# Optimization experiments

Measured on AMD Instinct MI355X. Metric: run time of the kernel, lower is better.

## Reference

```python
import jax, jax.numpy as jnp
import numpy as np

SATURATION = 1.0


def setup_inputs() -> dict:
    key = jax.random.key(0)
    k1, k2, k3, k4, k5 = jax.random.split(key, 5)
    B, Q, C = 128, 2048, 8
    L, K = 256, 64
    ts = jax.random.normal(k1, (B, Q, C), dtype=jnp.float32)
    shapelets = jax.random.normal(k2, (L, K, C), dtype=jnp.float32)  # stacked ParameterList
    gating = jax.random.normal(k3, (L,), dtype=jnp.float32)
    fc1_w = jax.random.normal(k4, (2, L), dtype=jnp.float32) / np.sqrt(L)
    fc1_b = jax.random.normal(k5, (2,), dtype=jnp.float32) * 0.01
    return {"ts": ts, "shapelets": shapelets, "gating": gating,
            "fc1_w": fc1_w, "fc1_b": fc1_b}


def reference(ts, shapelets, gating, fc1_w, fc1_b):
    # ts: [B, Q, C]; shapelets: [L, K, C]
    ts = ts.astype(jnp.float32)
    L, K, C = shapelets.shape
    # ||segment||^2 summed over (K, C) via sliding-window cumsum trick -> [B, S]
    ts2 = jnp.sum(ts * ts, axis=2)                     # [B, Q]
    csum = jnp.pad(jnp.cumsum(ts2, axis=1), ((0, 0), (1, 0)))
    win_sq = csum[:, K:] - csum[:, :-K]                # [B, S], S = Q-K+1
    # cross term <segment, shapelet> for all windows/shapelets via 1D conv
    kernel = jnp.transpose(shapelets, (1, 2, 0))       # [K, C, L] (WIO)
    cross = jax.lax.conv_general_dilated(
        ts, kernel, window_strides=(1,), padding='VALID',
        dimension_numbers=('NWC', 'WIO', 'NWC'))       # [B, S, L]
    sh_sq = jnp.sum(shapelets * shapelets, axis=(1, 2))  # [L]
    # mean squared distance per (batch, window, shapelet)
    dist = (win_sq[:, :, None] - 2.0 * cross + sh_sq[None, None, :]) / (K * C)
    hard_min = jnp.min(dist, axis=1)                   # [B, L] min-pool over windows
    g = jax.nn.sigmoid(SATURATION * gating)            # [L]
    min_dw = hard_min * g                              # equivalent to result @ diag(g)
    return min_dw @ fc1_w.T + fc1_b                    # [B, 2]
```

## Files before the change

kernel.cpp:

```cpp
#include <hip/hip_runtime.h>
#include <stdint.h>

#define B_ 128
#define Q_ 2048
#define C_ 8
#define L_ 256
#define K_ 64
#define S_ 1985
#define KC_ 512
#define BNC_ 64
#define NNT_ 4

typedef short s16x8 __attribute__((ext_vector_type(8)));
typedef float f32x16 __attribute__((ext_vector_type(16)));

__device__ __forceinline__ unsigned short f2bf(float f) {
    unsigned u = __float_as_uint(f);
    u += 0x7FFFu + ((u >> 16) & 1u);
    return (unsigned short)(u >> 16);
}
__device__ __forceinline__ unsigned fenc(float f) {
    unsigned u = __float_as_uint(f);
    return (u & 0x80000000u) ? ~u : (u | 0x80000000u);
}
__device__ __forceinline__ float fdec(unsigned k) {
    unsigned u = (k & 0x80000000u) ? (k ^ 0x80000000u) : ~k;
    return __uint_as_float(u);
}
__device__ __forceinline__ void async_copy16(void* lds_dst, const void* g_src) {
    __builtin_amdgcn_global_load_lds(
        (const __attribute__((address_space(1))) void*)g_src,
        (__attribute__((address_space(3))) void*)lds_dst, 16, 0, 0);
}

__global__ __launch_bounds__(256) void k_prep_ts(const float* __restrict__ ts,
                                                 uint4* __restrict__ tsb,
                                                 unsigned* __restrict__ extg) {
    const int b = blockIdx.x;
    const int t = threadIdx.x;
    __shared__ float t2[2048];
    #pragma unroll
    for (int j = 0; j < 8; ++j) {
        int r = j * 256 + t;
        const float4* p = (const float4*)(ts + ((size_t)b * Q_ + r) * C_);
        float4 x = p[0], y = p[1];
        union { unsigned short h[8]; uint4 v; } u;
        u.h[0] = f2bf(x.x); u.h[1] = f2bf(x.y); u.h[2] = f2bf(x.z); u.h[3] = f2bf(x.w);
        u.h[4] = f2bf(y.x); u.h[5] = f2bf(y.y); u.h[6] = f2bf(y.z); u.h[7] = f2bf(y.w);
        tsb[(size_t)b * Q_ + r] = u.v;
        t2[r] = x.x*x.x + x.y*x.y + x.z*x.z + x.w*x.w
              + y.x*y.x + y.y*y.y + y.z*y.z + y.w*y.w;
    }
    __syncthreads();
    int s0 = t * 8;
    float w = 0.f;
    if (s0 < S_) {
        #pragma unroll 16
        for (int k = 0; k < K_; ++k) w += t2[s0 + k];
    }
    #pragma unroll
    for (int j = 0; j < 8; ++j) {
        int s = s0 + j;
        unsigned word = 0x0000FF80u;
        if (s < S_) {
            float v = -0.5f * w;
            unsigned short hh = f2bf(v);
            float hf = __uint_as_float((unsigned)hh << 16);
            unsigned short ll = f2bf(v - hf);
            word = (unsigned)hh | ((unsigned)ll << 16);
        }
        extg[(size_t)b * Q_ + s] = word;
        if (s + K_ < Q_) w += t2[s + K_] - t2[s];
    }
}

__global__ __launch_bounds__(256) void k_misc(uint4* __restrict__ tsb,
                                              unsigned* __restrict__ hmin) {
    const int bid = blockIdx.x, t = threadIdx.x;
    if (bid < 2) {
        uint4 z; z.x = z.y = z.z = z.w = 0u;
        tsb[B_ * Q_ + bid * 256 + t] = z;
    } else {
        hmin[(bid - 2) * 256 + t] = 0xFFFFFFFFu;
    }
}

__global__ __launch_bounds__(64) void k_prep_sh(const float* __restrict__ sh,
                                                uint4* __restrict__ shb,
                                                float* __restrict__ shsq) {
    const int l = blockIdx.x;
    const int t = threadIdx.x;
    const float4* p = (const float4*)(sh + (size_t)l * KC_) + t * 2;
    float4 x = p[0], y = p[1];
    union { unsigned short h[8]; uint4 v; } u;
    u.h[0] = f2bf(x.x); u.h[1] = f2bf(x.y); u.h[2] = f2bf(x.z); u.h[3] = f2bf(x.w);
    u.h[4] = f2bf(y.x); u.h[5] = f2bf(y.y); u.h[6] = f2bf(y.z); u.h[7] = f2bf(y.w);
    shb[l * 64 + t] = u.v;
    float ss = x.x*x.x + x.y*x.y + x.z*x.z + x.w*x.w
             + y.x*y.x + y.y*y.y + y.z*y.z + y.w*y.w;
    #pragma unroll
    for (int off = 32; off >= 1; off >>= 1) ss += __shfl_down(ss, off, 64);
    if (t == 0) shsq[l] = ss;
}

__global__ __launch_bounds__(256, 2) void k_main(
    const uint4* __restrict__ tsb,
    const char*  __restrict__ shb,
    const unsigned* __restrict__ extg,
    const float* __restrict__ shsq,
    unsigned*    __restrict__ hmin)
{
    __shared__ uint4 b_lds4[4096];
    __shared__ uint4 a_lds4[576];
    __shared__ uint4 e_lds4[128];

    const int nt   = blockIdx.x;
    const int b    = blockIdx.y;
    const int c0   = nt * BNC_;
    const int tid  = threadIdx.x;
    const int lane = tid & 63;
    const int wv   = tid >> 6;
    const int l31  = lane & 31;
    const int hi   = lane >> 5;

    #define STAGE_AE(mi_)                                                      \
        {                                                                      \
            const char* gA = (const char*)(tsb + (size_t)b * Q_ + (mi_) * 512);\
            for (int rr = tid; rr < 576; rr += 256)                            \
                async_copy16((char*)a_lds4 + rr * 16, gA + rr * 16);           \
            if (tid < 128)                                                     \
                async_copy16((char*)e_lds4 + tid * 16,                         \
                             (const char*)(extg + (size_t)b * Q_ + (mi_) * 512)\
                             + tid * 16);                                      \
        }

    #pragma unroll
    for (int it = 0; it < 16; ++it) {
        int col  = wv * 16 + it;
        const char* g = shb + ((size_t)(c0 + col)) * 1024
                      + ((lane ^ (col & 31)) << 4);
        async_copy16((char*)b_lds4 + col * 1024, g);
    }
    STAGE_AE(0)
    __syncthreads();

    const f32x16 fz = {0.f,0.f,0.f,0.f,0.f,0.f,0.f,0.f,
                       0.f,0.f,0.f,0.f,0.f,0.f,0.f,0.f};
    const float inf = __builtin_inff();
    float rm0 = inf, rm1 = inf;

    const char* bb    = (const char*)b_lds4;
    const char* ab    = (const char*)a_lds4;
    const char* eb    = (const char*)e_lds4;
    const int   abase = (wv * 128 + l31 + hi) * 16;
    const int   bcol  = l31 * 1024;

    union UU { unsigned u[4]; s16x8 v; };
    UU be; be.u[0] = hi ? 0u : 0x3F803F80u;
    be.u[1] = 0u; be.u[2] = 0u; be.u[3] = 0u;

    #pragma unroll 1
    for (int mi = 0; mi < 4; ++mi) {
        f32x16 acc00 = fz, acc01 = fz;
        f32x16 acc10 = fz, acc11 = fz;
        f32x16 acc20 = fz, acc21 = fz;
        f32x16 acc30 = fz, acc31 = fz;

        #pragma unroll
        for (int kk = 0; kk < 32; ++kk) {
            s16x8 a0 = *(const s16x8*)(ab + abase + kk * 32);
            s16x8 a1 = *(const s16x8*)(ab + abase + kk * 32 + 512);
            s16x8 a2 = *(const s16x8*)(ab + abase + kk * 32 + 1024);
            s16x8 a3 = *(const s16x8*)(ab + abase + kk * 32 + 1536);
            int ch = (((kk << 1) + hi) ^ l31) << 4;
            s16x8 b0 = *(const s16x8*)(bb + bcol + ch);
            s16x8 b1 = *(const s16x8*)(bb + bcol + ch + 32768);
            __builtin_amdgcn_s_setprio(1);
            acc00 = __builtin_amdgcn_mfma_f32_32x32x16_bf16(a0, b0, acc00, 0, 0, 0);
            acc01 = __builtin_amdgcn_mfma_f32_32x32x16_bf16(a0, b1, acc01, 0, 0, 0);
            acc10 = __builtin_amdgcn_mfma_f32_32x32x16_bf16(a1, b0, acc10, 0, 0, 0);
            acc11 = __builtin_amdgcn_mfma_f32_32x32x16_bf16(a1, b1, acc11, 0, 0, 0);
            acc20 = __builtin_amdgcn_mfma_f32_32x32x16_bf16(a2, b0, acc20, 0, 0, 0);
            acc21 = __builtin_amdgcn_mfma_f32_32x32x16_bf16(a2, b1, acc21, 0, 0, 0);
            acc30 = __builtin_amdgcn_mfma_f32_32x32x16_bf16(a3, b0, acc30, 0, 0, 0);
            acc31 = __builtin_amdgcn_mfma_f32_32x32x16_bf16(a3, b1, acc31, 0, 0, 0);
            __builtin_amdgcn_s_setprio(0);
        }
        {
            unsigned w0 = *(const unsigned*)(eb + (wv * 128 +  0 + l31) * 4);
            unsigned w1 = *(const unsigned*)(eb + (wv * 128 + 32 + l31) * 4);
            unsigned w2 = *(const unsigned*)(eb + (wv * 128 + 64 + l31) * 4);
            unsigned w3 = *(const unsigned*)(eb + (wv * 128 + 96 + l31) * 4);
            UU ae0, ae1, ae2, ae3;
            ae0.u[0] = hi ? 0u : w0; ae0.u[1] = 0; ae0.u[2] = 0; ae0.u[3] = 0;
            ae1.u[0] = hi ? 0u : w1; ae1.u[1] = 0; ae1.u[2] = 0; ae1.u[3] = 0;
            ae2.u[0] = hi ? 0u : w2; ae2.u[1] = 0; ae2.u[2] = 0; ae2.u[3] = 0;
            ae3.u[0] = hi ? 0u : w3; ae3.u[1] = 0; ae3.u[2] = 0; ae3.u[3] = 0;
            acc00 = __builtin_amdgcn_mfma_f32_32x32x16_bf16(ae0.v, be.v, acc00, 0, 0, 0);
            acc01 = __builtin_amdgcn_mfma_f32_32x32x16_bf16(ae0.v, be.v, acc01, 0, 0, 0);
            acc10 = __builtin_amdgcn_mfma_f32_32x32x16_bf16(ae1.v, be.v, acc10, 0, 0, 0);
            acc11 = __builtin_amdgcn_mfma_f32_32x32x16_bf16(ae1.v, be.v, acc11, 0, 0, 0);
            acc20 = __builtin_amdgcn_mfma_f32_32x32x16_bf16(ae2.v, be.v, acc20, 0, 0, 0);
            acc21 = __builtin_amdgcn_mfma_f32_32x32x16_bf16(ae2.v, be.v, acc21, 0, 0, 0);
            acc30 = __builtin_amdgcn_mfma_f32_32x32x16_bf16(ae3.v, be.v, acc30, 0, 0, 0);
            acc31 = __builtin_amdgcn_mfma_f32_32x32x16_bf16(ae3.v, be.v, acc31, 0, 0, 0);
        }
        __syncthreads();
        if (mi < 3) STAGE_AE(mi + 1)

        #define FOLD(accv, rmv)                                                \
            { _Pragma("unroll") for (int r = 0; r < 16; ++r)                   \
                  rmv = fminf(rmv, -2.f * accv[r]); }
        FOLD(acc00, rm0) FOLD(acc10, rm0) FOLD(acc20, rm0) FOLD(acc30, rm0)
        FOLD(acc01, rm1) FOLD(acc11, rm1) FOLD(acc21, rm1) FOLD(acc31, rm1)
        #undef FOLD
        __syncthreads();
    }

    const int colg = c0 + l31;
    rm0 = (rm0 + shsq[colg])      * (1.f / 512.f);
    rm1 = (rm1 + shsq[colg + 32]) * (1.f / 512.f);
    rm0 = fminf(rm0, __shfl_xor(rm0, 32, 64));
    rm1 = fminf(rm1, __shfl_xor(rm1, 32, 64));
    if (hi == 0) {
        atomicMin(&hmin[b * L_ + colg],      fenc(rm0));
        atomicMin(&hmin[b * L_ + colg + 32], fenc(rm1));
    }
}

__global__ __launch_bounds__(256) void k_final(const unsigned* __restrict__ hmin,
                                               const float* __restrict__ gating,
                                               const float* __restrict__ w,
                                               const float* __restrict__ bias,
                                               float* __restrict__ out) {
    const int b = blockIdx.x, t = threadIdx.x;
    float v = fdec(hmin[b * L_ + t]);
    float g = 1.f / (1.f + __expf(-gating[t]));
    float mg = v * g;
    float p0 = mg * w[t];
    float p1 = mg * w[L_ + t];
    #pragma unroll
    for (int off = 32; off >= 1; off >>= 1) {
        p0 += __shfl_down(p0, off, 64);
        p1 += __shfl_down(p1, off, 64);
    }
    __shared__ float r0[4], r1[4];
    int wvi = t >> 6, ln = t & 63;
    if (ln == 0) { r0[wvi] = p0; r1[wvi] = p1; }
    __syncthreads();
    if (t == 0) {
        out[b * 2 + 0] = r0[0] + r0[1] + r0[2] + r0[3] + bias[0];
        out[b * 2 + 1] = r1[0] + r1[1] + r1[2] + r1[3] + bias[1];
    }
}

extern "C" void kernel_launch(void* const* d_in, const int* in_sizes, int n_in,
                              void* d_out, int out_size, void* d_ws, size_t ws_size,
                              hipStream_t stream) {
    const float* ts     = (const float*)d_in[0];
    const float* sh     = (const float*)d_in[1];
    const float* gating = (const float*)d_in[2];
    const float* fw     = (const float*)d_in[3];
    const float* fb     = (const float*)d_in[4];
    float* out = (float*)d_out;

    char* ws = (char*)d_ws;
    uint4*    tsb  = (uint4*)ws;
    char*     shb  = ws + 4202496;
    float*    shsq = (float*)(ws + 4464640);
    unsigned* hmin = (unsigned*)(ws + 4465664);
    unsigned* extg = (unsigned*)(ws + 4596736);

    k_prep_ts<<<128, 256, 0, stream>>>(ts, tsb, extg);
    k_misc<<<130, 256, 0, stream>>>(tsb, hmin);
    k_prep_sh<<<256, 64, 0, stream>>>(sh, (uint4*)shb, shsq);
    dim3 grid(NNT_, B_);
    k_main<<<grid, 256, 0, stream>>>(tsb, shb, extg, shsq, hmin);
    k_final<<<128, 256, 0, stream>>>(hmin, gating, fw, fb, out);
}
```

Baseline: 66.74 us.

## Retile main GEMM, stream shapelets from global, fuse prep kernels

Merges the three prep kernels into a single launch and stores the bf16 shapelets transposed so B fragments can be read straight from global memory. The main kernel's shared-memory B tile is removed. Its tiling changes from 4 column tiles by the full sequence per block to 256-row by 128-column tiles on a 16x128 grid. A double-buffered A tile replaces the old staging, and launch bounds rise to 3 blocks per CU. The aim is less LDS pressure and fewer launches plus higher occupancy, at the risk of extra L2 traffic for B and less reuse per block.

Result: slower. 194.3 us (+191.2%).

```diff
diff --git a/kernel.cpp b/kernel.cpp
--- a/kernel.cpp
+++ b/kernel.cpp
@@ -8,8 +8,6 @@
 #define K_ 64
 #define S_ 1985
 #define KC_ 512
-#define BNC_ 64
-#define NNT_ 4
 
 typedef short s16x8 __attribute__((ext_vector_type(8)));
 typedef float f32x16 __attribute__((ext_vector_type(16)));
@@ -33,115 +31,101 @@
         (__attribute__((address_space(3))) void*)lds_dst, 16, 0, 0);
 }
 
-__global__ __launch_bounds__(256) void k_prep_ts(const float* __restrict__ ts,
-                                                 uint4* __restrict__ tsb,
-                                                 unsigned* __restrict__ extg) {
-    const int b = blockIdx.x;
-    const int t = threadIdx.x;
+__global__ __launch_bounds__(256) void k_prep(const float* __restrict__ ts,
+                                              const float* __restrict__ sh,
+                                              uint4* __restrict__ tsb,
+                                              uint4* __restrict__ shb2,
+                                              float* __restrict__ shsq,
+                                              unsigned* __restrict__ extg,
+                                              unsigned* __restrict__ hmin) {
     __shared__ float t2[2048];
-    #pragma unroll
-    for (int j = 0; j < 8; ++j) {
-        int r = j * 256 + t;
-        const float4* p = (const float4*)(ts + ((size_t)b * Q_ + r) * C_);
+    const int bid = blockIdx.x, t = threadIdx.x;
+    if (bid < 128) {
+        const int b = bid;
+        #pragma unroll
+        for (int j = 0; j < 8; ++j) {
+            int r = j * 256 + t;
+            const float4* p = (const float4*)(ts + ((size_t)b * Q_ + r) * C_);
+            float4 x = p[0], y = p[1];
+            union { unsigned short h[8]; uint4 v; } u;
+            u.h[0] = f2bf(x.x); u.h[1] = f2bf(x.y); u.h[2] = f2bf(x.z); u.h[3] = f2bf(x.w);
+            u.h[4] = f2bf(y.x); u.h[5] = f2bf(y.y); u.h[6] = f2bf(y.z); u.h[7] = f2bf(y.w);
+            tsb[(size_t)b * Q_ + r] = u.v;
+            t2[r] = x.x*x.x + x.y*x.y + x.z*x.z + x.w*x.w
+                  + y.x*y.x + y.y*y.y + y.z*y.z + y.w*y.w;
+        }
+        __syncthreads();
+        int s0 = t * 8;
+        float w = 0.f;
+        if (s0 < S_) {
+            #pragma unroll 16
+            for (int k = 0; k < K_; ++k) w += t2[s0 + k];
+        }
+        #pragma unroll
+        for (int j = 0; j < 8; ++j) {
+            int s = s0 + j;
+            unsigned word = 0x0000FF80u;
+            if (s < S_) {
+                float v = -0.5f * w;
+                unsigned short hh = f2bf(v);
+                float hf = __uint_as_float((unsigned)hh << 16);
+                unsigned short ll = f2bf(v - hf);
+                word = (unsigned)hh | ((unsigned)ll << 16);
+            }
+            extg[(size_t)b * Q_ + s] = word;
+            if (s + K_ < Q_) w += t2[s + K_] - t2[s];
+        }
+    } else if (bid < 192) {
+        const int l = (bid - 128) * 4 + (t >> 6);
+        const int c = t & 63;
+        const float4* p = (const float4*)(sh + (size_t)l * KC_) + c * 2;
         float4 x = p[0], y = p[1];
         union { unsigned short h[8]; uint4 v; } u;
         u.h[0] = f2bf(x.x); u.h[1] = f2bf(x.y); u.h[2] = f2bf(x.z); u.h[3] = f2bf(x.w);
         u.h[4] = f2bf(y.x); u.h[5] = f2bf(y.y); u.h[6] = f2bf(y.z); u.h[7] = f2bf(y.w);
-        tsb[(size_t)b * Q_ + r] = u.v;
-        t2[r] = x.x*x.x + x.y*x.y + x.z*x.z + x.w*x.w
-              + y.x*y.x + y.y*y.y + y.z*y.z + y.w*y.w;
-    }
-    __syncthreads();
-    int s0 = t * 8;
-    float w = 0.f;
-    if (s0 < S_) {
-        #pragma unroll 16
-        for (int k = 0; k < K_; ++k) w += t2[s0 + k];
-    }
-    #pragma unroll
-    for (int j = 0; j < 8; ++j) {
-        int s = s0 + j;
-        unsigned word = 0x0000FF80u;
-        if (s < S_) {
-            float v = -0.5f * w;
-            unsigned short hh = f2bf(v);
-            float hf = __uint_as_float((unsigned)hh << 16);
-            unsigned short ll = f2bf(v - hf);
-            word = (unsigned)hh | ((unsigned)ll << 16);
-        }
-        extg[(size_t)b * Q_ + s] = word;
-        if (s + K_ < Q_) w += t2[s + K_] - t2[s];
-    }
-}
-
-__global__ __launch_bounds__(256) void k_misc(uint4* __restrict__ tsb,
-                                              unsigned* __restrict__ hmin) {
-    const int bid = blockIdx.x, t = threadIdx.x;
-    if (bid < 2) {
+        shb2[c * L_ + l] = u.v;
+        float ss = x.x*x.x + x.y*x.y + x.z*x.z + x.w*x.w
+                 + y.x*y.x + y.y*y.y + y.z*y.z + y.w*y.w;
+        #pragma unroll
+        for (int off = 32; off >= 1; off >>= 1) ss += __shfl_down(ss, off, 64);
+        if (c == 0) shsq[l] = ss;
+    } else if (bid < 194) {
         uint4 z; z.x = z.y = z.z = z.w = 0u;
-        tsb[B_ * Q_ + bid * 256 + t] = z;
+        tsb[B_ * Q_ + (bid - 192) * 256 + t] = z;
     } else {
-        hmin[(bid - 2) * 256 + t] = 0xFFFFFFFFu;
-    }
-}
-
-__global__ __launch_bounds__(64) void k_prep_sh(const float* __restrict__ sh,
-                                                uint4* __restrict__ shb,
-                                                float* __restrict__ shsq) {
-    const int l = blockIdx.x;
-    const int t = threadIdx.x;
-    const float4* p = (const float4*)(sh + (size_t)l * KC_) + t * 2;
-    float4 x = p[0], y = p[1];
-    union { unsigned short h[8]; uint4 v; } u;
-    u.h[0] = f2bf(x.x); u.h[1] = f2bf(x.y); u.h[2] = f2bf(x.z); u.h[3] = f2bf(x.w);
-    u.h[4] = f2bf(y.x); u.h[5] = f2bf(y.y); u.h[6] = f2bf(y.z); u.h[7] = f2bf(y.w);
-    shb[l * 64 + t] = u.v;
-    float ss = x.x*x.x + x.y*x.y + x.z*x.z + x.w*x.w
-             + y.x*y.x + y.y*y.y + y.z*y.z + y.w*y.w;
-    #pragma unroll
-    for (int off = 32; off >= 1; off >>= 1) ss += __shfl_down(ss, off, 64);
-    if (t == 0) shsq[l] = ss;
-}
-
-__global__ __launch_bounds__(256, 2) void k_main(
+        hmin[(bid - 194) * 256 + t] = 0xFFFFFFFFu;
+    }
+}
+
+__global__ __launch_bounds__(256, 3) void k_main(
     const uint4* __restrict__ tsb,
-    const char*  __restrict__ shb,
+    const uint4* __restrict__ shb2,
     const unsigned* __restrict__ extg,
     const float* __restrict__ shsq,
     unsigned*    __restrict__ hmin)
 {
-    __shared__ uint4 b_lds4[4096];
-    __shared__ uint4 a_lds4[576];
-    __shared__ uint4 e_lds4[128];
-
-    const int nt   = blockIdx.x;
+    __shared__ uint4 a_lds[2][192];
+
+    const int ms   = blockIdx.x >> 1;
+    const int nt   = blockIdx.x & 1;
     const int b    = blockIdx.y;
-    const int c0   = nt * BNC_;
+    const int m0   = ms * 256;
+    const int c0   = nt * 128;
     const int tid  = threadIdx.x;
     const int lane = tid & 63;
     const int wv   = tid >> 6;
     const int l31  = lane & 31;
     const int hi   = lane >> 5;
-
-    #define STAGE_AE(mi_)                                                      \
-        {                                                                      \
-            const char* gA = (const char*)(tsb + (size_t)b * Q_ + (mi_) * 512);\
-            for (int rr = tid; rr < 576; rr += 256)                            \
-                async_copy16((char*)a_lds4 + rr * 16, gA + rr * 16);           \
-            if (tid < 128)                                                     \
-                async_copy16((char*)e_lds4 + tid * 16,                         \
-                             (const char*)(extg + (size_t)b * Q_ + (mi_) * 512)\
-                             + tid * 16);                                      \
-        }
-
-    #pragma unroll
-    for (int it = 0; it < 16; ++it) {
-        int col  = wv * 16 + it;
-        const char* g = shb + ((size_t)(c0 + col)) * 1024
-                      + ((lane ^ (col & 31)) << 4);
-        async_copy16((char*)b_lds4 + col * 1024, g);
-    }
-    STAGE_AE(0)
+    const int wm   = wv >> 1;
+    const int wn   = wv & 1;
+
+    #define STAGE_A(p, mi_)                                                    \
+        if (tid < 192)                                                         \
+            async_copy16((char*)&a_lds[p][wv * 64] + lane * 16,                \
+                         (const char*)(tsb + (size_t)b * Q_ + m0 + (mi_) * 128)\
+                         + tid * 16);
+
+    STAGE_A(0, 0)
     __syncthreads();
 
     const f32x16 fz = {0.f,0.f,0.f,0.f,0.f,0.f,0.f,0.f,
@@ -149,75 +133,56 @@
     const float inf = __builtin_inff();
     float rm0 = inf, rm1 = inf;
 
-    const char* bb    = (const char*)b_lds4;
-    const char* ab    = (const char*)a_lds4;
-    const char* eb    = (const char*)e_lds4;
-    const int   abase = (wv * 128 + l31 + hi) * 16;
-    const int   bcol  = l31 * 1024;
+    const char* bbase = (const char*)shb2 + (size_t)(c0 + wn * 64 + l31) * 16;
+    const int   arow  = wm * 64 + l31 + hi;
 
     union UU { unsigned u[4]; s16x8 v; };
     UU be; be.u[0] = hi ? 0u : 0x3F803F80u;
     be.u[1] = 0u; be.u[2] = 0u; be.u[3] = 0u;
 
     #pragma unroll 1
-    for (int mi = 0; mi < 4; ++mi) {
+    for (int mi = 0; mi < 2; ++mi) {
+        const int p = mi & 1;
+        if (mi < 1) STAGE_A(p ^ 1, mi + 1)
+
         f32x16 acc00 = fz, acc01 = fz;
         f32x16 acc10 = fz, acc11 = fz;
-        f32x16 acc20 = fz, acc21 = fz;
-        f32x16 acc30 = fz, acc31 = fz;
-
+        const char* ab = (const char*)&a_lds[p][0];
         #pragma unroll
         for (int kk = 0; kk < 32; ++kk) {
-            s16x8 a0 = *(const s16x8*)(ab + abase + kk * 32);
-            s16x8 a1 = *(const s16x8*)(ab + abase + kk * 32 + 512);
-            s16x8 a2 = *(const s16x8*)(ab + abase + kk * 32 + 1024);
-            s16x8 a3 = *(const s16x8*)(ab + abase + kk * 32 + 1536);
-            int ch = (((kk << 1) + hi) ^ l31) << 4;
-            s16x8 b0 = *(const s16x8*)(bb + bcol + ch);
-            s16x8 b1 = *(const s16x8*)(bb + bcol + ch + 32768);
+            s16x8 a0 = *(const s16x8*)(ab + (arow + 2 * kk) * 16);
+            s16x8 a1 = *(const s16x8*)(ab + (arow + 32 + 2 * kk) * 16);
+            const char* bp = bbase + (size_t)(2 * kk + hi) * 4096;
+            s16x8 b0 = *(const s16x8*)(bp);
+            s16x8 b1 = *(const s16x8*)(bp + 512);
             __builtin_amdgcn_s_setprio(1);
             acc00 = __builtin_amdgcn_mfma_f32_32x32x16_bf16(a0, b0, acc00, 0, 0, 0);
             acc01 = __builtin_amdgcn_mfma_f32_32x32x16_bf16(a0, b1, acc01, 0, 0, 0);
             acc10 = __builtin_amdgcn_mfma_f32_32x32x16_bf16(a1, b0, acc10, 0, 0, 0);
             acc11 = __builtin_amdgcn_mfma_f32_32x32x16_bf16(a1, b1, acc11, 0, 0, 0);
-            acc20 = __builtin_amdgcn_mfma_f32_32x32x16_bf16(a2, b0, acc20, 0, 0, 0);
-            acc21 = __builtin_amdgcn_mfma_f32_32x32x16_bf16(a2, b1, acc21, 0, 0, 0);
-            acc30 = __builtin_amdgcn_mfma_f32_32x32x16_bf16(a3, b0, acc30, 0, 0, 0);
-            acc31 = __builtin_amdgcn_mfma_f32_32x32x16_bf16(a3, b1, acc31, 0, 0, 0);
             __builtin_amdgcn_s_setprio(0);
         }
         {
-            unsigned w0 = *(const unsigned*)(eb + (wv * 128 +  0 + l31) * 4);
-            unsigned w1 = *(const unsigned*)(eb + (wv * 128 + 32 + l31) * 4);
-            unsigned w2 = *(const unsigned*)(eb + (wv * 128 + 64 + l31) * 4);
-            unsigned w3 = *(const unsigned*)(eb + (wv * 128 + 96 + l31) * 4);
-            UU ae0, ae1, ae2, ae3;
+            size_t eb = (size_t)b * Q_ + m0 + mi * 128 + wm * 64 + l31;
+            unsigned w0 = extg[eb];
+            unsigned w1 = extg[eb + 32];
+            UU ae0, ae1;
             ae0.u[0] = hi ? 0u : w0; ae0.u[1] = 0; ae0.u[2] = 0; ae0.u[3] = 0;
             ae1.u[0] = hi ? 0u : w1; ae1.u[1] = 0; ae1.u[2] = 0; ae1.u[3] = 0;
-            ae2.u[0] = hi ? 0u : w2; ae2.u[1] = 0; ae2.u[2] = 0; ae2.u[3] = 0;
-            ae3.u[0] = hi ? 0u : w3; ae3.u[1] = 0; ae3.u[2] = 0; ae3.u[3] = 0;
             acc00 = __builtin_amdgcn_mfma_f32_32x32x16_bf16(ae0.v, be.v, acc00, 0, 0, 0);
             acc01 = __builtin_amdgcn_mfma_f32_32x32x16_bf16(ae0.v, be.v, acc01, 0, 0, 0);
             acc10 = __builtin_amdgcn_mfma_f32_32x32x16_bf16(ae1.v, be.v, acc10, 0, 0, 0);
             acc11 = __builtin_amdgcn_mfma_f32_32x32x16_bf16(ae1.v, be.v, acc11, 0, 0, 0);
-            acc20 = __builtin_amdgcn_mfma_f32_32x32x16_bf16(ae2.v, be.v, acc20, 0, 0, 0);
-            acc21 = __builtin_amdgcn_mfma_f32_32x32x16_bf16(ae2.v, be.v, acc21, 0, 0, 0);
-            acc30 = __builtin_amdgcn_mfma_f32_32x32x16_bf16(ae3.v, be.v, acc30, 0, 0, 0);
-            acc31 = __builtin_amdgcn_mfma_f32_32x32x16_bf16(ae3.v, be.v, acc31, 0, 0, 0);
+        }
+        #pragma unroll
+        for (int r = 0; r < 16; ++r) {
+            rm0 = fminf(rm0, fminf(-2.f * acc00[r], -2.f * acc10[r]));
+            rm1 = fminf(rm1, fminf(-2.f * acc01[r], -2.f * acc11[r]));
         }
         __syncthreads();
-        if (mi < 3) STAGE_AE(mi + 1)
-
-        #define FOLD(accv, rmv)                                                \
-            { _Pragma("unroll") for (int r = 0; r < 16; ++r)                   \
-                  rmv = fminf(rmv, -2.f * accv[r]); }
-        FOLD(acc00, rm0) FOLD(acc10, rm0) FOLD(acc20, rm0) FOLD(acc30, rm0)
-        FOLD(acc01, rm1) FOLD(acc11, rm1) FOLD(acc21, rm1) FOLD(acc31, rm1)
-        #undef FOLD
-        __syncthreads();
-    }
-
-    const int colg = c0 + l31;
+    }
+
+    const int colg = c0 + wn * 64 + l31;
     rm0 = (rm0 + shsq[colg])      * (1.f / 512.f);
     rm1 = (rm1 + shsq[colg + 32]) * (1.f / 512.f);
     rm0 = fminf(rm0, __shfl_xor(rm0, 32, 64));
@@ -266,15 +231,13 @@
 
     char* ws = (char*)d_ws;
     uint4*    tsb  = (uint4*)ws;
-    char*     shb  = ws + 4202496;
+    uint4*    shb2 = (uint4*)(ws + 4202496);
     float*    shsq = (float*)(ws + 4464640);
     unsigned* hmin = (unsigned*)(ws + 4465664);
     unsigned* extg = (unsigned*)(ws + 4596736);
 
-    k_prep_ts<<<128, 256, 0, stream>>>(ts, tsb, extg);
-    k_misc<<<130, 256, 0, stream>>>(tsb, hmin);
-    k_prep_sh<<<256, 64, 0, stream>>>(sh, (uint4*)shb, shsq);
-    dim3 grid(NNT_, B_);
-    k_main<<<grid, 256, 0, stream>>>(tsb, shb, extg, shsq, hmin);
+    k_prep<<<322, 256, 0, stream>>>(ts, sh, tsb, shb2, shsq, extg, hmin);
+    dim3 grid(16, B_);
+    k_main<<<grid, 256, 0, stream>>>(tsb, shb2, extg, shsq, hmin);
     k_final<<<128, 256, 0, stream>>>(hmin, gating, fw, fb, out);
 }
```
